# Kernel optimization log

Measured on AMD Instinct MI355X. Metric: run time of the kernel, lower is better.

## Reference

```python
import jax, jax.numpy as jnp
import numpy as np

B, T, N, H = 512, 128, 128, 256


def setup_inputs() -> dict:
    key = jax.random.key(0)
    ks = jax.random.split(key, 8)
    rn = lambda k, shape, sc: (jax.random.normal(k, shape, jnp.float32) * sc)
    return {
        "data": rn(ks[0], (B, T, N), 1.0),
        "h0": jnp.zeros((B, H), jnp.float32),
        # SimpleRNNCell params: h_t = tanh(x@Wx + h@Wh + b)
        "Wx": rn(ks[1], (N, H), 0.05),
        "Wh": rn(ks[2], (H, H), 0.05),
        "b": jnp.zeros((H,), jnp.float32),
        # InputAttention: w1: Dense(T) over last dim T; w2: Dense(T) over hidden; v: Dense(1)
        "W1": rn(ks[3], (T, T), 0.05),
        "b1": jnp.zeros((T,), jnp.float32),
        "W2": rn(ks[4], (H, T), 0.05),
        "b2": jnp.zeros((T,), jnp.float32),
        "Wv": rn(ks[5], (T, 1), 0.05),
        "bv": jnp.zeros((1,), jnp.float32),
        "n": N,
    }


def reference(data, h0, Wx, Wh, b, W1, b1, W2, b2, Wv, bv, n):
    # data: (B, T, n); h0: (B, H)
    Tlen = data.shape[1]
    x_perm = jnp.swapaxes(data, 1, 2)          # (B, n, T) == Permute((2,1))(x)
    pre = x_perm @ W1 + b1                      # w1(x_perm): loop-invariant, hoisted

    def step(h, x_t):
        # SimpleRNNCell: new state used for this step's attention
        h_new = jnp.tanh(x_t @ Wx + h @ Wh + b)                 # (B, H)
        q = h_new @ W2 + b2                                      # w2(RepeatVector(n)(h)) per row -> (B, T)
        score = jnp.tanh(pre + q[:, None, :])                    # (B, n, T)
        e = score @ Wv + bv                                      # (B, n, 1)
        e = jnp.swapaxes(e, 1, 2)                                # Permute((2,1)) -> (B, 1, n)
        alpha = jax.nn.softmax(e, axis=-1)                       # softmax over n
        return h_new, alpha

    xs = jnp.swapaxes(data, 0, 1)               # (T, B, n): data[:, t, :] per step
    _, alphas = jax.lax.scan(step, h0, xs)      # (T, B, 1, n)
    # faithful to tf.reshape(alpha_seq.stack(), (-1, T, n))
    alpha_seq = alphas.reshape(-1, Tlen, n)     # (B, T, n)
    return data * alpha_seq
```

## Files before the change

kernel.cpp:

```cpp
#include <hip/hip_runtime.h>


#define C2L 2.8853900817779268f
#define L2E 1.4426950408889634f

typedef _Float16 hf;
typedef _Float16 hf2 __attribute__((ext_vector_type(2)));
typedef _Float16 hf4 __attribute__((ext_vector_type(4)));
typedef _Float16 hf8 __attribute__((ext_vector_type(8)));
typedef float f32x4 __attribute__((ext_vector_type(4)));
typedef float f32x2 __attribute__((ext_vector_type(2)));

__device__ __forceinline__ float fast_exp2(float x){
#if __has_builtin(__builtin_amdgcn_exp2f)
  return __builtin_amdgcn_exp2f(x);
#else
  return exp2f(x);
#endif
}
__device__ __forceinline__ float fast_rcp(float x){
#if __has_builtin(__builtin_amdgcn_rcpf)
  return __builtin_amdgcn_rcpf(x);
#else
  return 1.f/x;
#endif
}
__device__ __forceinline__ f32x2 bc(float s){ return (f32x2){s, s}; }
__device__ __forceinline__ f32x2 fma2(f32x2 a, f32x2 b, f32x2 c){
  return __builtin_elementwise_fma(a, b, c);
}

__global__ __launch_bounds__(256) void k_prep_w(const float* __restrict__ Wx,
    const float* __restrict__ W2, const float* __restrict__ W1,
    hf* __restrict__ wts){
  int tid = blockIdx.x*256 + threadIdx.x;
  if (tid < 32768){
    int n = tid >> 7, k = tid & 127;
    wts[tid] = (hf)Wx[k*256 + n];
  } else if (tid < 65536){
    int t2 = tid - 32768;
    int n = t2 >> 8, k = t2 & 255;
    wts[tid] = (hf)W2[k*128 + n];
  } else {
    int t3 = tid - 65536;
    int n = t3 >> 7, k = t3 & 127;
    wts[tid] = (hf)W1[k*128 + n];
  }
}

template<int K, int MODE>
__global__ __launch_bounds__(256) void k_gemm(const void* __restrict__ Asrc,
    const hf* __restrict__ Bt, const float* __restrict__ bias,
    float* __restrict__ Cout){
  constexpr int SA = 136;
  __shared__ alignas(16) hf As[64*SA];
  __shared__ alignas(16) hf Bs[128*SA];
  const int tid = threadIdx.x;
  const int w = tid >> 6, lane = tid & 63;
  const int c = lane & 15, q = lane >> 4;
  const int bx = blockIdx.x;
  const int col0 = (MODE==0) ? blockIdx.y*128 : 0;

  float br[8];
  #pragma unroll
  for (int ni=0; ni<8; ni++) br[ni] = bias[col0 + ni*16 + c];

  f32x4 acc[8];
  #pragma unroll
  for (int ni=0; ni<8; ni++) acc[ni] = (f32x4){0.f,0.f,0.f,0.f};

  for (int kc=0; kc<K/128; kc++){
    if (MODE == 0){
      const float* A = (const float*)Asrc + (long)bx*64*128;
      #pragma unroll
      for (int v=0; v<8; v++){
        int f4 = v*256 + tid;
        int m = f4 >> 5, k4 = (f4 & 31)*4;
        float4 d = *(const float4*)&A[m*128 + k4];
        hf4 h = {(hf)d.x,(hf)d.y,(hf)d.z,(hf)d.w};
        *(hf4*)&As[m*SA + k4] = h;
      }
    } else if (MODE == 1){
      const hf* A = (const hf*)Asrc + (long)bx*64*256;
      #pragma unroll
      for (int v=0; v<4; v++){
        int f8 = v*256 + tid;
        int m = f8 >> 4, k8 = (f8 & 15)*8;
        *(hf8*)&As[m*SA + k8] = *(const hf8*)&A[m*256 + kc*128 + k8];
      }
    } else {
      const float* A = (const float*)Asrc + (long)(bx>>1)*16384;
      const int i0 = (bx & 1)*64;
      #pragma unroll
      for (int v=0; v<8; v++){
        int f4 = v*256 + tid;
        int t = f4 >> 4, i4 = (f4 & 15)*4;
        float4 d = *(const float4*)&A[t*128 + i0 + i4];
        As[(i4+0)*SA + t] = (hf)d.x;
        As[(i4+1)*SA + t] = (hf)d.y;
        As[(i4+2)*SA + t] = (hf)d.z;
        As[(i4+3)*SA + t] = (hf)d.w;
      }
    }
    #pragma unroll
    for (int v=0; v<8; v++){
      int f8 = v*256 + tid;
      int n = f8 >> 4, k8 = (f8 & 15)*8;
      *(hf8*)&Bs[n*SA + k8] = *(const hf8*)&Bt[(col0+n)*K + kc*128 + k8];
    }
    __syncthreads();
    #pragma unroll
    for (int kk=0; kk<4; kk++){
      hf8 a = *(const hf8*)&As[(w*16 + c)*SA + kk*32 + q*8];
      #pragma unroll
      for (int ni=0; ni<8; ni++){
        hf8 b = *(const hf8*)&Bs[(ni*16 + c)*SA + kk*32 + q*8];
        acc[ni] = __builtin_amdgcn_mfma_f32_16x16x32_f16(a, b, acc[ni], 0, 0, 0);
      }
    }
    __syncthreads();
  }
  #pragma unroll
  for (int ni=0; ni<8; ni++){
    #pragma unroll
    for (int r=0; r<4; r++){
      int rloc = w*16 + q*4 + r;
      int col = col0 + ni*16 + c;
      float val = acc[ni][r] + br[ni];
      int addr;
      if (MODE == 0){
        int R = bx*64 + rloc;
        int b_ = R >> 7, t_ = R & 127;
        addr = (t_*512 + b_)*256 + col;
      } else if (MODE == 1){
        int R = bx*64 + rloc;
        addr = R*128 + col;
        val = fast_exp2(C2L*val);
      } else {
        int b_ = bx >> 1, i_ = (bx & 1)*64 + rloc;
        addr = b_*16384 + i_*128 + col;
        val = fast_exp2(C2L*val);
      }
      Cout[addr] = val;
    }
  }
}

__global__ __launch_bounds__(1024, 4) void k_rnn(const float* __restrict__ h0,
    const float* __restrict__ Wh, const float* __restrict__ xw,
    hf* __restrict__ Hb){
  __shared__ alignas(16) char hs[2*8192];
  const int tid = threadIdx.x;
  const int w = tid >> 6, lane = tid & 63;
  const int c = lane & 15, q = lane >> 4;
  const int b0 = blockIdx.x * 16;
  const int col = w*16 + c;
  hf8 bw[8];
  #pragma unroll
  for (int kc=0; kc<8; kc++){
    #pragma unroll
    for (int e=0; e<8; e++){
      bw[kc][e] = (hf)Wh[(kc*32 + q*8 + e)*256 + col];
    }
  }
  if (tid < 512){
    int m = tid >> 5, s8 = tid & 31;
    const float* src = &h0[(b0 + m)*256 + s8*8];
    float4 d0 = *(const float4*)&src[0];
    float4 d1 = *(const float4*)&src[4];
    hf8 hv = {(hf)d0.x,(hf)d0.y,(hf)d0.z,(hf)d0.w,
              (hf)d1.x,(hf)d1.y,(hf)d1.z,(hf)d1.w};
    *(hf8*)&hs[m*512 + ((s8 ^ (m & 7)) << 4)] = hv;
  }
  float xwv[4];
  #pragma unroll
  for (int r=0; r<4; r++) xwv[r] = xw[(b0 + q*4 + r)*256 + col];
  __syncthreads();
  const int m = c;
  const int abase = m*512;
  for (int t=0; t<128; t++){
    const int p = t & 1;
    float xwn[4];
    if (t < 127){
      #pragma unroll
      for (int r=0; r<4; r++) xwn[r] = xw[((t+1)*512 + b0 + q*4 + r)*256 + col];
    } else {
      #pragma unroll
      for (int r=0; r<4; r++) xwn[r] = 0.f;
    }
    hf8 a[8];
    #pragma unroll
    for (int kc=0; kc<8; kc++)
      a[kc] = *(const hf8*)&hs[p*8192 + abase + ((((kc<<2)|q) ^ (m & 7)) << 4)];
    f32x4 acca = (f32x4){0.f,0.f,0.f,0.f};
    f32x4 accb = (f32x4){0.f,0.f,0.f,0.f};
    #pragma unroll
    for (int kc=0; kc<4; kc++){
      acca = __builtin_amdgcn_mfma_f32_16x16x32_f16(a[kc],   bw[kc],   acca, 0,0,0);
      accb = __builtin_amdgcn_mfma_f32_16x16x32_f16(a[kc+4], bw[kc+4], accb, 0,0,0);
    }
    #pragma unroll
    for (int r=0; r<4; r++){
      float v = acca[r] + accb[r] + xwv[r];
      float e2 = fast_exp2(v*C2L);
      float hn = 1.f - 2.f*fast_rcp(e2 + 1.f);
      int row = q*4 + r;
      *(hf*)&hs[(p^1)*8192 + row*512
                + (((col >> 3) ^ (row & 7)) << 4) + (col & 7)*2] = (hf)hn;
      Hb[(t*512 + b0 + row)*256 + col] = (hf)hn;
      xwv[r] = xwn[r];
    }
    __syncthreads();
  }
}

__global__ __launch_bounds__(512, 4) void k_attn(const float* __restrict__ P,
    const float* __restrict__ Qm, const float* __restrict__ Wv,
    const float* __restrict__ data, float* __restrict__ out){
  __shared__ alignas(16) float qs_t[128*36];
  __shared__ alignas(16) float wvs[128];
  __shared__ alignas(16) float epart[2][4][4][128];
  __shared__ float red[2][4][2];
  const int b = blockIdx.x, tile = blockIdx.y;
  const int tid = threadIdx.x;
  const int i = tid & 127, g = tid >> 7;
  const int t0 = tile*32;
  if (tid < 128) wvs[tid] = -2.f*Wv[tid];
  #pragma unroll
  for (int v=0; v<2; v++){
    int flat = v*2048 + tid*4;
    int tt = flat >> 7, c = flat & 127;
    float4 d = *(const float4*)&Qm[((t0+tt)*512 + b)*128 + c];
    qs_t[(c+0)*36 + tt] = d.x;
    qs_t[(c+1)*36 + tt] = d.y;
    qs_t[(c+2)*36 + tt] = d.z;
    qs_t[(c+3)*36 + tt] = d.w;
  }
  float4 p4[8];
  const float* prow = P + b*16384 + i*128 + g*32;
  #pragma unroll
  for (int v=0; v<8; v++) p4[v] = *(const float4*)&prow[v*4];
  __syncthreads();
  const f32x2 ONE2 = {1.f, 1.f};
  for (int tp=0; tp<8; tp++){
    const int pp = tp & 1;
    const float* qcol = &qs_t[(g*32)*36 + 4*tp];
    const float* wvr = &wvs[g*32];
    f32x2 ACC01 = {0.f,0.f}, ACC23 = {0.f,0.f};
    #pragma unroll
    for (int mm=0; mm<8; mm++){
      float4 qa = *(const float4*)&qcol[(mm*4+0)*36];
      float4 qb = *(const float4*)&qcol[(mm*4+1)*36];
      float4 qc = *(const float4*)&qcol[(mm*4+2)*36];
      float4 qd = *(const float4*)&qcol[(mm*4+3)*36];
      float4 Pv = p4[mm];
      float4 wv = *(const float4*)&wvr[mm*4];
      {
        f32x2 Qa = {qa.x, qa.y}, Qb = {qb.x, qb.y};
        f32x2 Qc = {qc.x, qc.y}, Qd = {qd.x, qd.y};
        f32x2 Ua = fma2(bc(Pv.x), Qa, ONE2);
        f32x2 Ub = fma2(bc(Pv.y), Qb, ONE2);
        f32x2 Uc = fma2(bc(Pv.z), Qc, ONE2);
        f32x2 Ud = fma2(bc(Pv.w), Qd, ONE2);
        f32x2 dab = Ua*Ub, dcd = Uc*Ud;
        f32x2 nab = fma2(bc(wv.x), Ub, bc(wv.y)*Ua);
        f32x2 ncd = fma2(bc(wv.z), Ud, bc(wv.w)*Uc);
        f32x2 D = dab*dcd;
        f32x2 N = fma2(nab, dcd, ncd*dab);
        f32x2 R = {fast_rcp(D.x), fast_rcp(D.y)};
        ACC01 = fma2(N, R, ACC01);
      }
      {
        f32x2 Qa = {qa.z, qa.w}, Qb = {qb.z, qb.w};
        f32x2 Qc = {qc.z, qc.w}, Qd = {qd.z, qd.w};
        f32x2 Ua = fma2(bc(Pv.x), Qa, ONE2);
        f32x2 Ub = fma2(bc(Pv.y), Qb, ONE2);
        f32x2 Uc = fma2(bc(Pv.z), Qc, ONE2);
        f32x2 Ud = fma2(bc(Pv.w), Qd, ONE2);
        f32x2 dab = Ua*Ub, dcd = Uc*Ud;
        f32x2 nab = fma2(bc(wv.x), Ub, bc(wv.y)*Ua);
        f32x2 ncd = fma2(bc(wv.z), Ud, bc(wv.w)*Uc);
        f32x2 D = dab*dcd;
        f32x2 N = fma2(nab, dcd, ncd*dab);
        f32x2 R = {fast_rcp(D.x), fast_rcp(D.y)};
        ACC23 = fma2(N, R, ACC23);
      }
    }
    epart[pp][g][0][i] = ACC01.x;
    epart[pp][g][1][i] = ACC01.y;
    epart[pp][g][2][i] = ACC23.x;
    epart[pp][g][3][i] = ACC23.y;
    __syncthreads();
    float e = epart[pp][0][g][i] + epart[pp][1][g][i]
            + epart[pp][2][g][i] + epart[pp][3][g][i];
    float pe = fast_exp2(e*L2E);
    float sm = pe;
    #pragma unroll
    for (int off=32; off; off>>=1) sm += __shfl_xor(sm, off);
    if ((tid & 63) == 0) red[pp][g][(tid>>6)&1] = sm;
    __syncthreads();
    float ssum = red[pp][g][0] + red[pp][g][1];
    float alpha = pe * fast_rcp(ssum);
    int t = t0 + 4*tp + g;
    int base = (t*512 + b)*128 + i;
    out[base] = data[base]*alpha;
  }
}

extern "C" void kernel_launch(void* const* d_in, const int* in_sizes, int n_in,
                              void* d_out, int out_size, void* d_ws, size_t ws_size,
                              hipStream_t stream) {
  const float* data = (const float*)d_in[0];
  const float* h0   = (const float*)d_in[1];
  const float* Wx   = (const float*)d_in[2];
  const float* Wh   = (const float*)d_in[3];
  const float* bb   = (const float*)d_in[4];
  const float* W1   = (const float*)d_in[5];
  const float* b1   = (const float*)d_in[6];
  const float* W2   = (const float*)d_in[7];
  const float* b2   = (const float*)d_in[8];
  const float* Wv   = (const float*)d_in[9];
  float* wsp = (float*)d_ws;
  float* P   = wsp;
  float* xwQ = wsp + 8388608;
  hf*    Hbf = (hf*)(wsp + 25165824);
  hf*    wts = (hf*)(wsp + 33554432);
  const hf* Wxt = wts;
  const hf* W2t = wts + 32768;
  const hf* W1t = wts + 65536;
  float* out = (float*)d_out;

  hipLaunchKernelGGL(k_prep_w, dim3(320), dim3(256), 0, stream, Wx, W2, W1, wts);
  hipLaunchKernelGGL((k_gemm<128,0>), dim3(1024,2), dim3(256), 0, stream,
                     (const void*)data, Wxt, bb, xwQ);
  hipLaunchKernelGGL((k_gemm<128,2>), dim3(1024),   dim3(256), 0, stream,
                     (const void*)data, W1t, b1, P);
  hipLaunchKernelGGL(k_rnn, dim3(32), dim3(1024), 0, stream, h0, Wh, xwQ, Hbf);
  hipLaunchKernelGGL((k_gemm<256,1>), dim3(1024),   dim3(256), 0, stream,
                     (const void*)Hbf, W2t, b2, xwQ);
  hipLaunchKernelGGL(k_attn, dim3(512, 4), dim3(512), 0, stream, P, xwQ, Wv, data, out);
}
```

Measured before the change: 363.8 us.

## Transpose Q via LDS in gemm epilogue, read Q uniformly in attn, halve RNN waves

The MODE 1 gemm now stages its output tile in shared memory and writes Q transposed per batch (b, tau, t), so k_attn can load Q with wave-uniform (readfirstlane) global loads instead of staging and transposing it through LDS. Wv is likewise loaded uniformly, and the -2 scale moves to the epilogue. The RNN kernel drops to 512 threads with each wave computing two 16-column tiles, prefetches xw two steps ahead, and writes Hb in (b, t) order to match the new gemm row mapping. These changes trade LDS traffic and a barrier in attn for scalar or uniform global loads, and trade fewer waves per step for more MFMA work per wave in the serial recurrence.

```diff
diff --git a/kernel.cpp b/kernel.cpp
--- a/kernel.cpp
+++ b/kernel.cpp
@@ -5,7 +5,6 @@
 #define L2E 1.4426950408889634f
 
 typedef _Float16 hf;
-typedef _Float16 hf2 __attribute__((ext_vector_type(2)));
 typedef _Float16 hf4 __attribute__((ext_vector_type(4)));
 typedef _Float16 hf8 __attribute__((ext_vector_type(8)));
 typedef float f32x4 __attribute__((ext_vector_type(4)));
@@ -28,6 +27,10 @@
 __device__ __forceinline__ f32x2 bc(float s){ return (f32x2){s, s}; }
 __device__ __forceinline__ f32x2 fma2(f32x2 a, f32x2 b, f32x2 c){
   return __builtin_elementwise_fma(a, b, c);
+}
+__device__ __forceinline__ float4 uld4(const float* __restrict__ p, int off){
+  off = __builtin_amdgcn_readfirstlane(off);
+  return *(const float4*)(p + off);
 }
 
 __global__ __launch_bounds__(256) void k_prep_w(const float* __restrict__ Wx,
@@ -53,8 +56,9 @@
     const hf* __restrict__ Bt, const float* __restrict__ bias,
     float* __restrict__ Cout){
   constexpr int SA = 136;
-  __shared__ alignas(16) hf As[64*SA];
-  __shared__ alignas(16) hf Bs[128*SA];
+  __shared__ alignas(16) char smem[64*SA*2 + 128*SA*2];
+  hf* As = (hf*)smem;
+  hf* Bs = (hf*)(smem + 64*SA*2);
   const int tid = threadIdx.x;
   const int w = tid >> 6, lane = tid & 63;
   const int c = lane & 15, q = lane >> 4;
@@ -120,33 +124,97 @@
     }
     __syncthreads();
   }
-  #pragma unroll
-  for (int ni=0; ni<8; ni++){
+  if (MODE == 1){
+    float* Cs = (float*)smem;
+    #pragma unroll
+    for (int ni=0; ni<8; ni++){
+      #pragma unroll
+      for (int r=0; r<4; r++){
+        int rloc = w*16 + q*4 + r;
+        Cs[rloc*129 + ni*16 + c] = acc[ni][r] + br[ni];
+      }
+    }
+    __syncthreads();
+    const int b_  = bx >> 1;
+    const int t0_ = (bx & 1) * 64;
+    const int tq  = (tid & 15) * 4;
+    #pragma unroll
+    for (int jj=0; jj<8; jj++){
+      int tau = jj*16 + (tid >> 4);
+      float4 o;
+      o.x = fast_exp2(C2L * Cs[(tq+0)*129 + tau]);
+      o.y = fast_exp2(C2L * Cs[(tq+1)*129 + tau]);
+      o.z = fast_exp2(C2L * Cs[(tq+2)*129 + tau]);
+      o.w = fast_exp2(C2L * Cs[(tq+3)*129 + tau]);
+      *(float4*)&Cout[((long)b_*128 + tau)*128 + t0_ + tq] = o;
+    }
+  } else {
+    #pragma unroll
+    for (int ni=0; ni<8; ni++){
+      #pragma unroll
+      for (int r=0; r<4; r++){
+        int rloc = w*16 + q*4 + r;
+        int col = col0 + ni*16 + c;
+        float val = acc[ni][r] + br[ni];
+        int addr;
+        if (MODE == 0){
+          int R = bx*64 + rloc;
+          int b2_ = R >> 7, t2_ = R & 127;
+          addr = (t2_*512 + b2_)*256 + col;
+        } else {
+          int b2_ = bx >> 1, i_ = (bx & 1)*64 + rloc;
+          addr = b2_*16384 + i_*128 + col;
+          val = fast_exp2(C2L*val);
+        }
+        Cout[addr] = val;
+      }
+    }
+  }
+}
+
+__device__ __forceinline__ void rnn_step(int T, int b0, int w0, int c, int q,
+    char* hs, const hf8 (&bw)[2][8], float (&buf)[2][4],
+    const float* __restrict__ xw, hf* __restrict__ Hb){
+  const int p = T & 1;
+  const int abase = c*512;
+  hf8 a[8];
+  #pragma unroll
+  for (int kc=0; kc<8; kc++)
+    a[kc] = *(const hf8*)&hs[p*8192 + abase + ((((kc<<2)|q) ^ (c & 7)) << 4)];
+  f32x4 ac0a = (f32x4){0.f,0.f,0.f,0.f}, ac0b = ac0a;
+  f32x4 ac1a = ac0a, ac1b = ac0a;
+  #pragma unroll
+  for (int kc=0; kc<4; kc++){
+    ac0a = __builtin_amdgcn_mfma_f32_16x16x32_f16(a[kc],   bw[0][kc],   ac0a,0,0,0);
+    ac0b = __builtin_amdgcn_mfma_f32_16x16x32_f16(a[kc+4], bw[0][kc+4], ac0b,0,0,0);
+    ac1a = __builtin_amdgcn_mfma_f32_16x16x32_f16(a[kc],   bw[1][kc],   ac1a,0,0,0);
+    ac1b = __builtin_amdgcn_mfma_f32_16x16x32_f16(a[kc+4], bw[1][kc+4], ac1b,0,0,0);
+  }
+  #pragma unroll
+  for (int nt=0; nt<2; nt++){
     #pragma unroll
     for (int r=0; r<4; r++){
-      int rloc = w*16 + q*4 + r;
-      int col = col0 + ni*16 + c;
-      float val = acc[ni][r] + br[ni];
-      int addr;
-      if (MODE == 0){
-        int R = bx*64 + rloc;
-        int b_ = R >> 7, t_ = R & 127;
-        addr = (t_*512 + b_)*256 + col;
-      } else if (MODE == 1){
-        int R = bx*64 + rloc;
-        addr = R*128 + col;
-        val = fast_exp2(C2L*val);
-      } else {
-        int b_ = bx >> 1, i_ = (bx & 1)*64 + rloc;
-        addr = b_*16384 + i_*128 + col;
-        val = fast_exp2(C2L*val);
-      }
-      Cout[addr] = val;
-    }
-  }
-}
-
-__global__ __launch_bounds__(1024, 4) void k_rnn(const float* __restrict__ h0,
+      float v = (nt ? (ac1a[r]+ac1b[r]) : (ac0a[r]+ac0b[r])) + buf[nt][r];
+      float e2 = fast_exp2(v*C2L);
+      float hn = 1.f - 2.f*fast_rcp(e2 + 1.f);
+      int row = q*4 + r;
+      int col = w0 + nt*16 + c;
+      *(hf*)&hs[(p^1)*8192 + row*512
+                + (((col >> 3) ^ (row & 7)) << 4) + (col & 7)*2] = (hf)hn;
+      Hb[((long)(b0 + row)*128 + T)*256 + col] = (hf)hn;
+    }
+  }
+  #pragma unroll
+  for (int nt=0; nt<2; nt++){
+    #pragma unroll
+    for (int r=0; r<4; r++){
+      buf[nt][r] = (T+2 < 128)
+        ? xw[((T+2)*512 + b0 + q*4 + r)*256 + w0 + nt*16 + c] : 0.f;
+    }
+  }
+}
+
+__global__ __launch_bounds__(512, 2) void k_rnn(const float* __restrict__ h0,
     const float* __restrict__ Wh, const float* __restrict__ xw,
     hf* __restrict__ Hb){
   __shared__ alignas(16) char hs[2*8192];
@@ -154,16 +222,19 @@
   const int w = tid >> 6, lane = tid & 63;
   const int c = lane & 15, q = lane >> 4;
   const int b0 = blockIdx.x * 16;
-  const int col = w*16 + c;
-  hf8 bw[8];
-  #pragma unroll
-  for (int kc=0; kc<8; kc++){
-    #pragma unroll
-    for (int e=0; e<8; e++){
-      bw[kc][e] = (hf)Wh[(kc*32 + q*8 + e)*256 + col];
-    }
-  }
-  if (tid < 512){
+  const int w0 = w * 32;
+  hf8 bw[2][8];
+  #pragma unroll
+  for (int nt=0; nt<2; nt++){
+    #pragma unroll
+    for (int kc=0; kc<8; kc++){
+      #pragma unroll
+      for (int e=0; e<8; e++){
+        bw[nt][kc][e] = (hf)Wh[(kc*32 + q*8 + e)*256 + w0 + nt*16 + c];
+      }
+    }
+  }
+  {
     int m = tid >> 5, s8 = tid & 31;
     const float* src = &h0[(b0 + m)*256 + s8*8];
     float4 d0 = *(const float4*)&src[0];
@@ -172,89 +243,54 @@
               (hf)d1.x,(hf)d1.y,(hf)d1.z,(hf)d1.w};
     *(hf8*)&hs[m*512 + ((s8 ^ (m & 7)) << 4)] = hv;
   }
-  float xwv[4];
-  #pragma unroll
-  for (int r=0; r<4; r++) xwv[r] = xw[(b0 + q*4 + r)*256 + col];
+  float bufA[2][4], bufB[2][4];
+  #pragma unroll
+  for (int nt=0; nt<2; nt++){
+    #pragma unroll
+    for (int r=0; r<4; r++){
+      bufA[nt][r] = xw[(0*512 + b0 + q*4 + r)*256 + w0 + nt*16 + c];
+      bufB[nt][r] = xw[(1*512 + b0 + q*4 + r)*256 + w0 + nt*16 + c];
+    }
+  }
   __syncthreads();
-  const int m = c;
-  const int abase = m*512;
-  for (int t=0; t<128; t++){
-    const int p = t & 1;
-    float xwn[4];
-    if (t < 127){
-      #pragma unroll
-      for (int r=0; r<4; r++) xwn[r] = xw[((t+1)*512 + b0 + q*4 + r)*256 + col];
-    } else {
-      #pragma unroll
-      for (int r=0; r<4; r++) xwn[r] = 0.f;
-    }
-    hf8 a[8];
-    #pragma unroll
-    for (int kc=0; kc<8; kc++)
-      a[kc] = *(const hf8*)&hs[p*8192 + abase + ((((kc<<2)|q) ^ (m & 7)) << 4)];
-    f32x4 acca = (f32x4){0.f,0.f,0.f,0.f};
-    f32x4 accb = (f32x4){0.f,0.f,0.f,0.f};
-    #pragma unroll
-    for (int kc=0; kc<4; kc++){
-      acca = __builtin_amdgcn_mfma_f32_16x16x32_f16(a[kc],   bw[kc],   acca, 0,0,0);
-      accb = __builtin_amdgcn_mfma_f32_16x16x32_f16(a[kc+4], bw[kc+4], accb, 0,0,0);
-    }
-    #pragma unroll
-    for (int r=0; r<4; r++){
-      float v = acca[r] + accb[r] + xwv[r];
-      float e2 = fast_exp2(v*C2L);
-      float hn = 1.f - 2.f*fast_rcp(e2 + 1.f);
-      int row = q*4 + r;
-      *(hf*)&hs[(p^1)*8192 + row*512
-                + (((col >> 3) ^ (row & 7)) << 4) + (col & 7)*2] = (hf)hn;
-      Hb[(t*512 + b0 + row)*256 + col] = (hf)hn;
-      xwv[r] = xwn[r];
-    }
+  for (int t=0; t<128; t+=2){
+    rnn_step(t,   b0, w0, c, q, hs, bw, bufA, xw, Hb);
+    __syncthreads();
+    rnn_step(t+1, b0, w0, c, q, hs, bw, bufB, xw, Hb);
     __syncthreads();
   }
 }
 
 __global__ __launch_bounds__(512, 4) void k_attn(const float* __restrict__ P,
-    const float* __restrict__ Qm, const float* __restrict__ Wv,
+    const float* __restrict__ Qt, const float* __restrict__ Wv,
     const float* __restrict__ data, float* __restrict__ out){
-  __shared__ alignas(16) float qs_t[128*36];
-  __shared__ alignas(16) float wvs[128];
   __shared__ alignas(16) float epart[2][4][4][128];
   __shared__ float red[2][4][2];
   const int b = blockIdx.x, tile = blockIdx.y;
   const int tid = threadIdx.x;
   const int i = tid & 127, g = tid >> 7;
   const int t0 = tile*32;
-  if (tid < 128) wvs[tid] = -2.f*Wv[tid];
-  #pragma unroll
-  for (int v=0; v<2; v++){
-    int flat = v*2048 + tid*4;
-    int tt = flat >> 7, c = flat & 127;
-    float4 d = *(const float4*)&Qm[((t0+tt)*512 + b)*128 + c];
-    qs_t[(c+0)*36 + tt] = d.x;
-    qs_t[(c+1)*36 + tt] = d.y;
-    qs_t[(c+2)*36 + tt] = d.z;
-    qs_t[(c+3)*36 + tt] = d.w;
-  }
   float4 p4[8];
   const float* prow = P + b*16384 + i*128 + g*32;
   #pragma unroll
   for (int v=0; v<8; v++) p4[v] = *(const float4*)&prow[v*4];
-  __syncthreads();
+  float4 wvv[8];
+  #pragma unroll
+  for (int mm=0; mm<8; mm++) wvv[mm] = uld4(Wv, g*32 + mm*4);
+  const int qbase = (b*128 + g*32)*128 + t0;
   const f32x2 ONE2 = {1.f, 1.f};
   for (int tp=0; tp<8; tp++){
     const int pp = tp & 1;
-    const float* qcol = &qs_t[(g*32)*36 + 4*tp];
-    const float* wvr = &wvs[g*32];
+    const int qo = qbase + 4*tp;
     f32x2 ACC01 = {0.f,0.f}, ACC23 = {0.f,0.f};
     #pragma unroll
     for (int mm=0; mm<8; mm++){
-      float4 qa = *(const float4*)&qcol[(mm*4+0)*36];
-      float4 qb = *(const float4*)&qcol[(mm*4+1)*36];
-      float4 qc = *(const float4*)&qcol[(mm*4+2)*36];
-      float4 qd = *(const float4*)&qcol[(mm*4+3)*36];
+      float4 qa = uld4(Qt, qo + (mm*4+0)*128);
+      float4 qb = uld4(Qt, qo + (mm*4+1)*128);
+      float4 qc = uld4(Qt, qo + (mm*4+2)*128);
+      float4 qd = uld4(Qt, qo + (mm*4+3)*128);
       float4 Pv = p4[mm];
-      float4 wv = *(const float4*)&wvr[mm*4];
+      float4 wv = wvv[mm];
       {
         f32x2 Qa = {qa.x, qa.y}, Qb = {qb.x, qb.y};
         f32x2 Qc = {qc.x, qc.y}, Qd = {qd.x, qd.y};
@@ -286,10 +322,10 @@
         ACC23 = fma2(N, R, ACC23);
       }
     }
-    epart[pp][g][0][i] = ACC01.x;
-    epart[pp][g][1][i] = ACC01.y;
-    epart[pp][g][2][i] = ACC23.x;
-    epart[pp][g][3][i] = ACC23.y;
+    epart[pp][g][0][i] = -2.f*ACC01.x;
+    epart[pp][g][1][i] = -2.f*ACC01.y;
+    epart[pp][g][2][i] = -2.f*ACC23.x;
+    epart[pp][g][3][i] = -2.f*ACC23.y;
     __syncthreads();
     float e = epart[pp][0][g][i] + epart[pp][1][g][i]
             + epart[pp][2][g][i] + epart[pp][3][g][i];
@@ -321,7 +357,7 @@
   const float* b2   = (const float*)d_in[8];
   const float* Wv   = (const float*)d_in[9];
   float* wsp = (float*)d_ws;
-  float* P   = wsp;
+  float* Pm  = wsp;
   float* xwQ = wsp + 8388608;
   hf*    Hbf = (hf*)(wsp + 25165824);
   hf*    wts = (hf*)(wsp + 33554432);
@@ -334,9 +370,9 @@
   hipLaunchKernelGGL((k_gemm<128,0>), dim3(1024,2), dim3(256), 0, stream,
                      (const void*)data, Wxt, bb, xwQ);
   hipLaunchKernelGGL((k_gemm<128,2>), dim3(1024),   dim3(256), 0, stream,
-                     (const void*)data, W1t, b1, P);
-  hipLaunchKernelGGL(k_rnn, dim3(32), dim3(1024), 0, stream, h0, Wh, xwQ, Hbf);
+                     (const void*)data, W1t, b1, Pm);
+  hipLaunchKernelGGL(k_rnn, dim3(32), dim3(512), 0, stream, h0, Wh, xwQ, Hbf);
   hipLaunchKernelGGL((k_gemm<256,1>), dim3(1024),   dim3(256), 0, stream,
                      (const void*)Hbf, W2t, b2, xwQ);
-  hipLaunchKernelGGL(k_attn, dim3(512, 4), dim3(512), 0, stream, P, xwQ, Wv, data, out);
-}
+  hipLaunchKernelGGL(k_attn, dim3(512, 4), dim3(512), 0, stream, Pm, xwQ, Wv, data, out);
+}
```

Result: slower. 413.7 us (+13.7%).
